# Kernel tuning notes

Measured on AMD Instinct MI355X. Metric: run time of the kernel, lower is better.

Reference implementation:

```python
import jax, jax.numpy as jnp
import numpy as np

H, D = 16, 64  # heads, dim_head


def _rope(x):
    # x: (b, h, n, d). rotary-embedding-torch style: interleaved pairs, theta=10000.
    n, d = x.shape[-2], x.shape[-1]
    inv_freq = 1.0 / (10000.0 ** (jnp.arange(0, d, 2, dtype=jnp.float32) / d))  # (d/2,)
    ang = jnp.arange(n, dtype=jnp.float32)[:, None] * inv_freq[None, :]  # (n, d/2)
    cos = jnp.repeat(jnp.cos(ang), 2, axis=-1).astype(x.dtype)  # (n, d) interleaved
    sin = jnp.repeat(jnp.sin(ang), 2, axis=-1).astype(x.dtype)
    xp = x.reshape(*x.shape[:-1], d // 2, 2)
    rot = jnp.stack((-xp[..., 1], xp[..., 0]), axis=-1).reshape(x.shape)
    return x * cos + rot * sin


def setup_inputs() -> dict:
    key = jax.random.key(0)
    k1, k2, k3 = jax.random.split(key, 3)
    b, n, dim = 2, 2048, 1024
    inner = H * D
    x = jax.random.normal(k1, (b, n, dim), jnp.float32)
    w_qkv = jax.random.normal(k2, (dim, 3 * inner), jnp.float32) / np.sqrt(dim).astype(np.float32)
    w_out = jax.random.normal(k3, (inner, dim), jnp.float32) / np.sqrt(inner).astype(np.float32)
    b_out = jnp.zeros((dim,), jnp.float32)
    return {"x": x, "w_qkv": w_qkv, "w_out": w_out, "b_out": b_out}


def reference(x, w_qkv, w_out, b_out):
    b, n, _ = x.shape
    qkv = x @ w_qkv  # (b, n, 3*H*D)
    q, k, v = jnp.split(qkv, 3, axis=-1)

    def split_heads(t):
        return t.reshape(b, n, H, D).transpose(0, 2, 1, 3)  # (b, h, n, d)

    q, k, v = split_heads(q), split_heads(k), split_heads(v)
    q = _rope(q)
    k = _rope(k)
    scale = 1.0 / jnp.sqrt(jnp.asarray(D, dtype=x.dtype))
    scores = jnp.einsum('bhqd,bhkd->bhqk', q, k) * scale
    attn = jax.nn.softmax(scores, axis=-1)
    o = jnp.einsum('bhqk,bhkd->bhqd', attn, v)
    o = o.transpose(0, 2, 1, 3).reshape(b, n, H * D)
    return o @ w_out + b_out
```

## Files before the change

kernel.cpp:

```cpp
#include <hip/hip_runtime.h>
#include <math.h>

#define B_    2
#define N_    2048
#define DIM_  1024
#define H_    16
#define D_    64
#define INNER_ 1024
#define QKVC_ 3072

typedef __attribute__((ext_vector_type(8))) short short8;
typedef __attribute__((ext_vector_type(4))) short short4v;
typedef __attribute__((ext_vector_type(4))) float f32x4;
typedef __attribute__((ext_vector_type(4))) float float4v;
typedef _Float16 half8 __attribute__((ext_vector_type(8)));
typedef __fp16 fp16v2 __attribute__((ext_vector_type(2)));

union h8u { short8 s; half8 h; fp16v2 h2[4]; };
static __device__ __forceinline__ half8 s2h(short8 s) { h8u u; u.s = s; return u.h; }

static __device__ __forceinline__ unsigned short f2h(float f) {
    _Float16 h = (_Float16)f;
    unsigned short u;
    __builtin_memcpy(&u, &h, 2);
    return u;
}

static __device__ __forceinline__ void gload16(const void* g, void* l) {
    __builtin_amdgcn_global_load_lds((__attribute__((address_space(1))) void*)(g),
                                     (__attribute__((address_space(3))) void*)(l),
                                     16, 0, 0);
}

__global__ __launch_bounds__(256) void convert_all(const float* __restrict__ X,
                                                   const float* __restrict__ Wq,
                                                   const float* __restrict__ Wo,
                                                   unsigned short* __restrict__ Xh,
                                                   unsigned short* __restrict__ WqT,
                                                   unsigned short* __restrict__ WoT) {
    __shared__ unsigned short Sh[64][65];
    const int blk = blockIdx.x;
    const int tid = threadIdx.x;
    if (blk < 2048) {
        int t = blk * 256 + tid;
        size_t off = (size_t)t * 8;
        float4v a = *(const float4v*)(X + off);
        float4v b = *(const float4v*)(X + off + 4);
        short8 o;
#pragma unroll
        for (int j = 0; j < 4; ++j) {
            o[j]     = (short)f2h(a[j]);
            o[4 + j] = (short)f2h(b[j]);
        }
        *(short8*)(Xh + off) = o;
        return;
    }
    const float* W;
    unsigned short* T;
    int n0, k0, Nw;
    if (blk < 2816) {
        int g = blk - 2048;
        W = Wq; T = WqT; Nw = QKVC_;
        n0 = (g % 48) * 64; k0 = (g / 48) * 64;
    } else {
        int g = blk - 2816;
        W = Wo; T = WoT; Nw = DIM_;
        n0 = (g % 16) * 64; k0 = (g / 16) * 64;
    }
#pragma unroll
    for (int l = 0; l < 16; ++l) {
        int idx = tid + l * 256;
        int r = idx >> 6, c = idx & 63;
        Sh[c][r] = f2h(W[(size_t)(k0 + r) * Nw + n0 + c]);
    }
    __syncthreads();
#pragma unroll
    for (int l = 0; l < 16; ++l) {
        int idx = tid + l * 256;
        int r = idx >> 6, c = idx & 63;
        T[(size_t)(n0 + r) * 1024 + k0 + c] = Sh[r][c];
    }
}

#define GEMM_STAGE_H(gA, gB)                                                       \
    {                                                                              \
        int rr0 = w * 32 + (lane >> 2), rr1 = w * 32 + 16 + (lane >> 2);           \
        int kc = (lane & 3) * 8;                                                   \
        gload16(gA + (size_t)(m0 + rr0) * 1024 + k0 + kc, sA + (w * 32) * 32);     \
        gload16(gA + (size_t)(m0 + rr1) * 1024 + k0 + kc, sA + (w * 32 + 16) * 32);\
        gload16(gB + (size_t)(n0 + rr0) * 1024 + k0 + kc, sB + (w * 32) * 32);     \
        gload16(gB + (size_t)(n0 + rr1) * 1024 + k0 + kc, sB + (w * 32 + 16) * 32);\
    }

#define GEMM_BODY_H()                                                              \
    half8 af[4], bf[4];                                                            \
    _Pragma("unroll") for (int f = 0; f < 4; ++f) {                                \
        af[f] = s2h(*(const short8*)&sA[(wr + f * 16 + (lane & 15)) * 32 + (lane >> 4) * 8]); \
        bf[f] = s2h(*(const short8*)&sB[(wc + f * 16 + (lane & 15)) * 32 + (lane >> 4) * 8]); \
    }                                                                              \
    _Pragma("unroll") for (int i = 0; i < 4; ++i)                                  \
        _Pragma("unroll") for (int j = 0; j < 4; ++j)                              \
            acc[i][j] = __builtin_amdgcn_mfma_f32_16x16x32_f16(af[i], bf[j], acc[i][j], 0, 0, 0);

#define XCD_REMAP()                                                                \
    const int fblk = blockIdx.y * gridDim.x + blockIdx.x;                          \
    const int per_ = (gridDim.x * gridDim.y) >> 3;                                 \
    const int rf = (fblk & 7) * per_ + (fblk >> 3);                                \
    const int m0 = (rf / gridDim.x) * 128, n0 = (rf % gridDim.x) * 128;

#define QSCALE 0.180336879963f
__global__ __launch_bounds__(256) void qkv_gemm_mfma(const unsigned short* __restrict__ Ah,
                                                     const unsigned short* __restrict__ Bh,
                                                     unsigned short* __restrict__ Qh,
                                                     unsigned short* __restrict__ Kh,
                                                     unsigned short* __restrict__ Vh) {
    __shared__ __align__(16) unsigned short sA[4096], sB[4096];
    const int tid = threadIdx.x;
    const int lane = tid & 63, w = tid >> 6;
    const int wr = (w >> 1) * 64, wc = (w & 1) * 64;
    XCD_REMAP();
    f32x4 acc[4][4] = {};

    for (int k0 = 0; k0 < 1024; k0 += 32) {
        GEMM_STAGE_H(Ah, Bh);
        __syncthreads();
        GEMM_BODY_H();
        __syncthreads();
    }

    const int seg = n0 >> 10;
    const int parity = lane & 1;

#pragma unroll
    for (int i = 0; i < 4; ++i) {
        int mbase = m0 + wr + i * 16 + (lane >> 4) * 4;
#pragma unroll
        for (int j = 0; j < 4; ++j) {
            int col = n0 + wc + j * 16 + (lane & 15);
            int wcol = col & 1023;
            int h = wcol >> 6, dd = wcol & 63;
            unsigned short* dst = (seg == 0) ? Qh : (seg == 1 ? Kh : Vh);
            if (seg == 2) {
#pragma unroll
                for (int r = 0; r < 4; ++r) {
                    int row = mbase + r;
                    int b = row >> 11, n = row & (N_ - 1);
                    dst[((size_t)(b * H_ + h) * N_ + n) * D_ + dd] = f2h(acc[i][j][r]);
                }
            } else {
                float freq = __builtin_amdgcn_exp2f((float)(dd >> 1) * -0.4152410118f);
#pragma unroll
                for (int r = 0; r < 4; ++r) {
                    int row = mbase + r;
                    int b = row >> 11, n = row & (N_ - 1);
                    float ang = (float)n * freq;
                    float s = __sinf(ang);
                    float c = __cosf(ang);
                    float val = acc[i][j][r];
                    float partner = __shfl_xor(val, 1);
                    float rot = parity ? (val * c + partner * s)
                                       : (val * c - partner * s);
                    if (seg == 0) rot *= QSCALE;
                    dst[((size_t)(b * H_ + h) * N_ + n) * D_ + dd] = f2h(rot);
                }
            }
        }
    }
}

__global__ __launch_bounds__(256) void out_gemm_mfma(const unsigned short* __restrict__ Ah,
                                                     const unsigned short* __restrict__ Bh,
                                                     const float* __restrict__ bias,
                                                     float* __restrict__ C) {
    __shared__ __align__(16) unsigned short sA[4096], sB[4096];
    const int tid = threadIdx.x;
    const int lane = tid & 63, w = tid >> 6;
    const int wr = (w >> 1) * 64, wc = (w & 1) * 64;
    XCD_REMAP();
    f32x4 acc[4][4] = {};

    for (int k0 = 0; k0 < 1024; k0 += 32) {
        GEMM_STAGE_H(Ah, Bh);
        __syncthreads();
        GEMM_BODY_H();
        __syncthreads();
    }

#pragma unroll
    for (int i = 0; i < 4; ++i) {
        int mbase = m0 + wr + i * 16 + (lane >> 4) * 4;
#pragma unroll
        for (int j = 0; j < 4; ++j) {
            int col = n0 + wc + j * 16 + (lane & 15);
            float bv = bias[col];
#pragma unroll
            for (int r = 0; r < 4; ++r)
                C[(size_t)(mbase + r) * DIM_ + col] = acc[i][j][r] + bv;
        }
    }
}

#define PADV 72
#define NT   (N_ / 64)
__global__ __launch_bounds__(512, 4) void attn_mfma(const unsigned short* __restrict__ Qh,
                                                    const unsigned short* __restrict__ Kh,
                                                    const unsigned short* __restrict__ Vh,
                                                    unsigned short* __restrict__ Oh) {
    __shared__ __align__(16) unsigned short Ks[2 * 64 * 64];
    __shared__ __align__(16) unsigned short Vt[3][64][PADV];
    const int tid = threadIdx.x;
    const int w = tid >> 6;
    const int l = tid & 63;
    const int lr = l & 15, lg = l >> 4;

    const int f = blockIdx.y * gridDim.x + blockIdx.x;
    const int x = f & 7, g = f >> 3;
    const int bh = x * 4 + (g >> 4);
    const int q0 = (g & 15) * 128;
    const size_t base = (size_t)bh * N_ * D_;

    const int srow = tid >> 3;
    const int scg  = tid & 7;
    const int gcg  = scg ^ (srow & 7);
    const unsigned short* ksrc = Kh + base + (size_t)srow * D_ + gcg * 8;
    unsigned short* kdst = Ks + w * 512;

    const int kb0 = lr * 64 + (lg ^ (lr & 7)) * 8;
    const int kb1 = lr * 64 + ((lg + 4) ^ (lr & 7)) * 8;

    const int sd0 = (tid & 15) * 4;
    const int skv = (tid >> 4) * 2;
    const int vpos = ((skv >> 5) * 32) + (((skv >> 2) & 3) * 8) +
                     (((skv >> 4) & 1) * 4) + (skv & 3);

    const unsigned short* qrow = Qh + base + (size_t)(q0 + w * 16 + lr) * D_ + lg * 8;
    const half8 qf0 = s2h(*(const short8*)qrow);
    const half8 qf1 = s2h(*(const short8*)(qrow + 32));

    f32x4 oacc[4] = {};
    float lsum = 0.f;
    h8u pa_prev[2];
    pa_prev[0].s = short8{0,0,0,0,0,0,0,0};
    pa_prev[1].s = short8{0,0,0,0,0,0,0,0};

    gload16(ksrc, kdst);
    {
        short4v r0 = *(const short4v*)(Vh + base + (size_t)(skv + 0) * D_ + sd0);
        short4v r1 = *(const short4v*)(Vh + base + (size_t)(skv + 1) * D_ + sd0);
#pragma unroll
        for (int j = 0; j < 4; ++j) {
            unsigned int pk = (unsigned int)(unsigned short)r0[j] |
                              ((unsigned int)(unsigned short)r1[j] << 16);
            *(unsigned int*)&Vt[0][sd0 + j][vpos] = pk;
        }
    }

    int rd = 2, cu = 0, wr_ = 1;

    for (int ti = 0; ti < NT; ++ti) {
        const int kcur = ti & 1, knxt = kcur ^ 1;
        __syncthreads();

        short4v n0v = {}, n1v = {};
        if (ti + 1 < NT) {
            gload16(ksrc + (size_t)(ti + 1) * 64 * D_, kdst + knxt * 4096);
            const unsigned short* nsrc = Vh + base + (size_t)((ti + 1) * 64 + skv) * D_ + sd0;
            n0v = *(const short4v*)nsrc;
            n1v = *(const short4v*)(nsrc + D_);
        }

        f32x4 sacc[4] = {};
        const unsigned short* kbuf = Ks + kcur * 4096;
        __builtin_amdgcn_s_setprio(1);
#pragma unroll
        for (int t = 0; t < 4; ++t) {
            half8 kf0 = s2h(*(const short8*)(kbuf + t * 1024 + kb0));
            half8 kf1 = s2h(*(const short8*)(kbuf + t * 1024 + kb1));
            sacc[t] = __builtin_amdgcn_mfma_f32_16x16x32_f16(kf0, qf0, sacc[t], 0, 0, 0);
            sacc[t] = __builtin_amdgcn_mfma_f32_16x16x32_f16(kf1, qf1, sacc[t], 0, 0, 0);
        }
        if (ti > 0) {
#pragma unroll
            for (int m2 = 0; m2 < 2; ++m2)
#pragma unroll
                for (int dt = 0; dt < 4; ++dt) {
                    half8 vf = s2h(*(const short8*)&Vt[rd][dt * 16 + lr][m2 * 32 + lg * 8]);
                    oacc[dt] = __builtin_amdgcn_mfma_f32_16x16x32_f16(pa_prev[m2].h, vf, oacc[dt], 0, 0, 0);
                }
        }
        __builtin_amdgcn_s_setprio(0);

#pragma unroll
        for (int t = 0; t < 4; ++t) {
            float e0 = __builtin_amdgcn_exp2f(sacc[t][0]);
            float e1 = __builtin_amdgcn_exp2f(sacc[t][1]);
            float e2 = __builtin_amdgcn_exp2f(sacc[t][2]);
            float e3 = __builtin_amdgcn_exp2f(sacc[t][3]);
            lsum += (e0 + e1) + (e2 + e3);
            pa_prev[t >> 1].h2[(t & 1) * 2]     = __builtin_amdgcn_cvt_pkrtz(e0, e1);
            pa_prev[t >> 1].h2[(t & 1) * 2 + 1] = __builtin_amdgcn_cvt_pkrtz(e2, e3);
        }

        if (ti + 1 < NT) {
#pragma unroll
            for (int j = 0; j < 4; ++j) {
                unsigned int pk = (unsigned int)(unsigned short)n0v[j] |
                                  ((unsigned int)(unsigned short)n1v[j] << 16);
                *(unsigned int*)&Vt[wr_][sd0 + j][vpos] = pk;
            }
        }
        int t_ = rd; rd = cu; cu = wr_; wr_ = t_;
    }

#pragma unroll
    for (int m2 = 0; m2 < 2; ++m2)
#pragma unroll
        for (int dt = 0; dt < 4; ++dt) {
            half8 vf = s2h(*(const short8*)&Vt[rd][dt * 16 + lr][m2 * 32 + lg * 8]);
            oacc[dt] = __builtin_amdgcn_mfma_f32_16x16x32_f16(pa_prev[m2].h, vf, oacc[dt], 0, 0, 0);
        }

    lsum += __shfl_xor(lsum, 16);
    lsum += __shfl_xor(lsum, 32);
    int b = bh >> 4, h = bh & 15;
#pragma unroll
    for (int r = 0; r < 4; ++r) {
        float ls = __shfl(lsum, lg * 4 + r);
        float inv = 1.0f / ls;
        size_t orow = ((size_t)b * N_ + q0 + w * 16 + lg * 4 + r) * INNER_ + h * 64 + lr;
#pragma unroll
        for (int dt = 0; dt < 4; ++dt)
            Oh[orow + 16 * dt] = f2h(oacc[dt][r] * inv);
    }
}

extern "C" void kernel_launch(void* const* d_in, const int* in_sizes, int n_in,
                              void* d_out, int out_size, void* d_ws, size_t ws_size,
                              hipStream_t stream) {
    const float* x     = (const float*)d_in[0];
    const float* w_qkv = (const float*)d_in[1];
    const float* w_out = (const float*)d_in[2];
    const float* b_out = (const float*)d_in[3];
    float* out = (float*)d_out;

    unsigned short* Xh  = (unsigned short*)d_ws;
    unsigned short* WqT = Xh + 4194304;
    unsigned short* WoT = WqT + 3145728;
    unsigned short* Qh  = WoT + 1048576;
    unsigned short* Kh  = Qh + 4194304;
    unsigned short* Vh  = Kh + 4194304;

    convert_all<<<dim3(3072), 256, 0, stream>>>(x, w_qkv, w_out, Xh, WqT, WoT);
    qkv_gemm_mfma<<<dim3(QKVC_ / 128, 32), 256, 0, stream>>>(Xh, WqT, Qh, Kh, Vh);
    attn_mfma<<<dim3(N_ / 128, B_ * H_), 512, 0, stream>>>(Qh, Kh, Vh, Xh);
    out_gemm_mfma<<<dim3(DIM_ / 128, 32), 256, 0, stream>>>(Xh, WoT, b_out, out);
}
```

Before: 121.3 us.

## Double GEMM K-tile to 64 with XOR-swizzled LDS layout

Both the QKV and output GEMM kernels now stage 64-wide K slices instead of 32, which halves the number of loop iterations and barrier pairs. Each K step issues two MFMAs per accumulator. The LDS layout uses an XOR swizzle on 16-byte chunks, applied in both the global-to-LDS writes and the fragment reads, to avoid bank conflicts with the wider 128-byte rows. LDS use per block doubles to 32 KB, which may lower occupancy.

```diff
diff --git a/kernel.cpp b/kernel.cpp
--- a/kernel.cpp
+++ b/kernel.cpp
@@ -82,25 +82,34 @@
     }
 }
 
-#define GEMM_STAGE_H(gA, gB)                                                       \
+#define GEMM_STAGE64(gA, gB)                                                       \
     {                                                                              \
-        int rr0 = w * 32 + (lane >> 2), rr1 = w * 32 + 16 + (lane >> 2);           \
-        int kc = (lane & 3) * 8;                                                   \
-        gload16(gA + (size_t)(m0 + rr0) * 1024 + k0 + kc, sA + (w * 32) * 32);     \
-        gload16(gA + (size_t)(m0 + rr1) * 1024 + k0 + kc, sA + (w * 32 + 16) * 32);\
-        gload16(gB + (size_t)(n0 + rr0) * 1024 + k0 + kc, sB + (w * 32) * 32);     \
-        gload16(gB + (size_t)(n0 + rr1) * 1024 + k0 + kc, sB + (w * 32 + 16) * 32);\
-    }
-
-#define GEMM_BODY_H()                                                              \
-    half8 af[4], bf[4];                                                            \
+        int srow = lane >> 3;                                                      \
+        int gsw  = ((lane & 7) ^ srow) * 8;                                        \
+        _Pragma("unroll") for (int i_ = 0; i_ < 4; ++i_) {                         \
+            gload16(gA + (size_t)(m0 + w * 32 + 8 * i_ + srow) * 1024 + k0 + gsw,  \
+                    sA + (w * 32 + 8 * i_) * 64);                                  \
+            gload16(gB + (size_t)(n0 + w * 32 + 8 * i_ + srow) * 1024 + k0 + gsw,  \
+                    sB + (w * 32 + 8 * i_) * 64);                                  \
+        }                                                                          \
+    }
+
+#define GEMM_BODY64()                                                              \
+    half8 af[4][2], bf[4][2];                                                      \
     _Pragma("unroll") for (int f = 0; f < 4; ++f) {                                \
-        af[f] = s2h(*(const short8*)&sA[(wr + f * 16 + (lane & 15)) * 32 + (lane >> 4) * 8]); \
-        bf[f] = s2h(*(const short8*)&sB[(wc + f * 16 + (lane & 15)) * 32 + (lane >> 4) * 8]); \
+        int arow = (wr + f * 16 + (lane & 15)) * 64;                               \
+        int brow = (wc + f * 16 + (lane & 15)) * 64;                               \
+        _Pragma("unroll") for (int h = 0; h < 2; ++h) {                            \
+            int g = (((lane >> 4) + 4 * h) ^ (lane & 7)) * 8;                      \
+            af[f][h] = s2h(*(const short8*)&sA[arow + g]);                         \
+            bf[f][h] = s2h(*(const short8*)&sB[brow + g]);                         \
+        }                                                                          \
     }                                                                              \
     _Pragma("unroll") for (int i = 0; i < 4; ++i)                                  \
-        _Pragma("unroll") for (int j = 0; j < 4; ++j)                              \
-            acc[i][j] = __builtin_amdgcn_mfma_f32_16x16x32_f16(af[i], bf[j], acc[i][j], 0, 0, 0);
+        _Pragma("unroll") for (int j = 0; j < 4; ++j) {                            \
+            acc[i][j] = __builtin_amdgcn_mfma_f32_16x16x32_f16(af[i][0], bf[j][0], acc[i][j], 0, 0, 0); \
+            acc[i][j] = __builtin_amdgcn_mfma_f32_16x16x32_f16(af[i][1], bf[j][1], acc[i][j], 0, 0, 0); \
+        }
 
 #define XCD_REMAP()                                                                \
     const int fblk = blockIdx.y * gridDim.x + blockIdx.x;                          \
@@ -114,17 +123,17 @@
                                                      unsigned short* __restrict__ Qh,
                                                      unsigned short* __restrict__ Kh,
                                                      unsigned short* __restrict__ Vh) {
-    __shared__ __align__(16) unsigned short sA[4096], sB[4096];
+    __shared__ __align__(16) unsigned short sA[8192], sB[8192];
     const int tid = threadIdx.x;
     const int lane = tid & 63, w = tid >> 6;
     const int wr = (w >> 1) * 64, wc = (w & 1) * 64;
     XCD_REMAP();
     f32x4 acc[4][4] = {};
 
-    for (int k0 = 0; k0 < 1024; k0 += 32) {
-        GEMM_STAGE_H(Ah, Bh);
-        __syncthreads();
-        GEMM_BODY_H();
+    for (int k0 = 0; k0 < 1024; k0 += 64) {
+        GEMM_STAGE64(Ah, Bh);
+        __syncthreads();
+        GEMM_BODY64();
         __syncthreads();
     }
 
@@ -172,17 +181,17 @@
                                                      const unsigned short* __restrict__ Bh,
                                                      const float* __restrict__ bias,
                                                      float* __restrict__ C) {
-    __shared__ __align__(16) unsigned short sA[4096], sB[4096];
+    __shared__ __align__(16) unsigned short sA[8192], sB[8192];
     const int tid = threadIdx.x;
     const int lane = tid & 63, w = tid >> 6;
     const int wr = (w >> 1) * 64, wc = (w & 1) * 64;
     XCD_REMAP();
     f32x4 acc[4][4] = {};
 
-    for (int k0 = 0; k0 < 1024; k0 += 32) {
-        GEMM_STAGE_H(Ah, Bh);
-        __syncthreads();
-        GEMM_BODY_H();
+    for (int k0 = 0; k0 < 1024; k0 += 64) {
+        GEMM_STAGE64(Ah, Bh);
+        __syncthreads();
+        GEMM_BODY64();
         __syncthreads();
     }
 
```

After: 120.3 us. No clear change (-0.8%).
